# Optimization experiments

Hardware: AMD Instinct MI355X
Metric: run time of the kernel (lower is better)

Reference implementation:

```python
import jax, jax.numpy as jnp
import numpy as np

CENTER_RADIUS = 2.5
TOPK = 13
IOU_WEIGHT = 3.0
BETA = 2.0
NUM_CLASSES = 80
BBOX_W = 2.0
BIG = 1e8
EPS = 1e-7
IMG = 1280


def pairwise_iou(boxes, gts):
    # boxes [N,4], gts [M,4] xyxy -> [N,M]
    lt = jnp.maximum(boxes[:, None, :2], gts[None, :, :2])
    rb = jnp.minimum(boxes[:, None, 2:], gts[None, :, 2:])
    wh = jnp.clip(rb - lt, 0.0)
    inter = wh[..., 0] * wh[..., 1]
    area_a = (boxes[:, 2] - boxes[:, 0]) * (boxes[:, 3] - boxes[:, 1])
    area_b = (gts[:, 2] - gts[:, 0]) * (gts[:, 3] - gts[:, 1])
    union = area_a[:, None] + area_b[None, :] - inter
    return inter / jnp.maximum(union, EPS)


def giou_elementwise(a, b):
    # a,b [N,4] xyxy -> [N]
    lt = jnp.maximum(a[:, :2], b[:, :2])
    rb = jnp.minimum(a[:, 2:], b[:, 2:])
    wh = jnp.clip(rb - lt, 0.0)
    inter = wh[:, 0] * wh[:, 1]
    area_a = (a[:, 2] - a[:, 0]) * (a[:, 3] - a[:, 1])
    area_b = (b[:, 2] - b[:, 0]) * (b[:, 3] - b[:, 1])
    union = area_a + area_b - inter
    iou = inter / jnp.maximum(union, EPS)
    elt = jnp.minimum(a[:, :2], b[:, :2])
    erb = jnp.maximum(a[:, 2:], b[:, 2:])
    ewh = jnp.clip(erb - elt, 0.0)
    enclose = ewh[:, 0] * ewh[:, 1]
    return iou - (enclose - union) / jnp.maximum(enclose, EPS)


def simota_assign(pred_scores, pred_boxes, points, strides, gt_boxes, gt_labels):
    N = points.shape[0]
    M = gt_boxes.shape[0]
    px, py = points[:, 0], points[:, 1]
    # Step 1: candidate selection (inside box OR inside center region)
    in_box = ((px[:, None] > gt_boxes[None, :, 0]) & (py[:, None] > gt_boxes[None, :, 1]) &
              (px[:, None] < gt_boxes[None, :, 2]) & (py[:, None] < gt_boxes[None, :, 3]))
    gcx = (gt_boxes[:, 0] + gt_boxes[:, 2]) * 0.5
    gcy = (gt_boxes[:, 1] + gt_boxes[:, 3]) * 0.5
    r = CENTER_RADIUS * strides[:, None]
    in_center = ((px[:, None] > gcx[None, :] - r) & (py[:, None] > gcy[None, :] - r) &
                 (px[:, None] < gcx[None, :] + r) & (py[:, None] < gcy[None, :] + r))
    is_cand = in_box | in_center          # [N,M]
    cand_any = is_cand.any(axis=1)        # [N]
    # Step 2: cost = BCE(prob, onehot) + w * (-log IoU)
    iou = pairwise_iou(pred_boxes, gt_boxes)  # [N,M]
    p = jnp.clip(pred_scores, 1e-6, 1.0 - 1e-6)
    log_p = jnp.log(p)
    log_1mp = jnp.log1p(-p)
    all_neg = -log_1mp.sum(axis=-1)       # [N] sum_c BCE(p_c, 0)
    cls_cost = all_neg[:, None] + log_1mp[:, gt_labels] - log_p[:, gt_labels]
    reg_cost = -jnp.log(iou + EPS)
    cost = cls_cost + IOU_WEIGHT * reg_cost
    cost = jnp.where(is_cand, cost, BIG)
    # Step 3: dynamic k from top-k IoUs over candidate points (candidates of any gt)
    iou_cand = jnp.where(cand_any[:, None], iou, 0.0)
    topk_ious, _ = jax.lax.top_k(iou_cand.T, TOPK)            # [M,TOPK]
    dyn_k = jnp.clip(topk_ious.sum(axis=-1).astype(jnp.int32), 1, None)  # [M], <= TOPK
    # Step 4: per-gt lowest-cost candidates; k_j entries, only valid (cost < BIG)
    neg_top, top_idx = jax.lax.top_k(-cost.T, TOPK)           # [M,TOPK]
    top_cost = -neg_top
    ranks = jnp.arange(TOPK)
    select = (ranks[None, :] < dyn_k[:, None]) & (top_cost < BIG)
    matching = jnp.zeros((N, M), bool).at[top_idx, jnp.arange(M)[:, None]].set(select)
    # Step 5: conflict resolution -> keep lowest-cost gt per point
    matched = matching.any(axis=1)
    best = jnp.argmin(jnp.where(matching, cost, jnp.inf), axis=1)  # [N]
    rows = jnp.arange(N)
    labels = jnp.where(matched, gt_labels[best], NUM_CLASSES)
    aboxes = jnp.where(matched[:, None], gt_boxes[best], 0.0)
    pos_iou = jnp.where(matched, iou[rows, best], 0.0)
    ascores = jnp.zeros((N, NUM_CLASSES), pred_scores.dtype).at[rows, gt_labels[best]].set(pos_iou)
    return labels, aboxes, ascores


def reference(pred_logits, pred_boxes, points, strides, gt_boxes, gt_labels):
    pred_scores = jax.nn.sigmoid(pred_logits)
    sg = jax.lax.stop_gradient
    labels, aboxes, ascores = simota_assign(sg(pred_scores), sg(pred_boxes),
                                            sg(points), sg(strides), sg(gt_boxes), gt_labels)
    labels, aboxes, ascores = sg(labels), sg(aboxes), sg(ascores)
    # Quality Focal Loss
    x, t = pred_logits, ascores
    bce = jnp.maximum(x, 0.0) - x * t + jnp.log1p(jnp.exp(-jnp.abs(x)))
    scale = jnp.abs(t - pred_scores) ** BETA
    n_pos_cls = jnp.maximum(1, (t > 0).sum()).astype(x.dtype)
    loss_cls = (scale * bce).sum() / n_pos_cls
    # GIoU loss over positives
    matched = labels < NUM_CLASSES
    g = giou_elementwise(pred_boxes, aboxes)
    n_pos = jnp.maximum(1, matched.sum()).astype(x.dtype)
    loss_box = jnp.where(matched, 1.0 - g, 0.0).sum() / n_pos
    return loss_cls + BBOX_W * loss_box


def setup_inputs() -> dict:
    key = jax.random.key(0)
    k1, k2, k3, k4, k5 = jax.random.split(key, 5)
    # multi-scale grid points for a 1280x1280 image, strides 8/16/32
    pts, strs = [], []
    for s in (8, 16, 32):
        n = IMG // s
        c = (jnp.arange(n, dtype=jnp.float32) + 0.5) * s
        yy, xx = jnp.meshgrid(c, c, indexing='ij')
        pts.append(jnp.stack([xx.ravel(), yy.ravel()], axis=-1))
        strs.append(jnp.full((n * n,), float(s), jnp.float32))
    points = jnp.concatenate(pts, axis=0)          # [33600,2]
    strides = jnp.concatenate(strs, axis=0)        # [33600]
    N = points.shape[0]
    pred_logits = jax.random.normal(k1, (N, NUM_CLASSES), jnp.float32) - 2.0
    # decode-style boxes: point +/- positive ltrb distances
    d = jax.random.uniform(k2, (N, 4), jnp.float32) * 64.0 + 1.0
    pred_boxes = jnp.stack([points[:, 0] - d[:, 0], points[:, 1] - d[:, 1],
                            points[:, 0] + d[:, 2], points[:, 1] + d[:, 3]], axis=-1)
    M = 256
    c = jax.random.uniform(k3, (M, 2), jnp.float32) * IMG
    wh = jax.random.uniform(k4, (M, 2), jnp.float32) * 200.0 + 8.0
    gt_boxes = jnp.concatenate([jnp.clip(c - wh / 2, 0, IMG), jnp.clip(c + wh / 2, 0, IMG)], axis=-1)
    gt_labels = jax.random.randint(k5, (M,), 0, NUM_CLASSES, jnp.int32)
    return {"pred_logits": pred_logits, "pred_boxes": pred_boxes, "points": points,
            "strides": strides, "gt_boxes": gt_boxes, "gt_labels": gt_labels}
```

## Files before the change

kernel.cpp:

```cpp
#include <hip/hip_runtime.h>
#include <cstdint>
#include <math.h>

#define NCLS 80
#define TKK 13
#define BIGC 100000000.0f
#define EPSC 1e-7f
#define CRAD 2.5f
#define MARGIN 66.0f
#define XCLP 13.815511f
#define AW 8

__device__ __constant__ int   c_ln[3]   = {160, 80, 40};
__device__ __constant__ float c_ls[3]   = {8.0f, 16.0f, 32.0f};
__device__ __constant__ int   c_lbase[3]= {0, 25600, 32000};

__device__ __forceinline__ void sig_sp(float x, float& s, float& sp){
    float e = __expf(-fabsf(x));
    float L = __logf(1.0f + e);
    sp = fmaxf(x, 0.0f) + L;
    s = __fdividef((x >= 0.0f) ? 1.0f : e, 1.0f + e);
}

__global__ __launch_bounds__(256) void k_prep(
    const float* __restrict__ logits, const float* __restrict__ gt,
    int M, int N, int nbA,
    unsigned long long* __restrict__ best, char* __restrict__ cand,
    float* __restrict__ comb_t, double* __restrict__ base_cls,
    double* __restrict__ accd, int* __restrict__ acci)
{
    int b = blockIdx.x;
    if (b < nbA){
        __shared__ float t[64][81];
        __shared__ float s_an[64];
        int tid = threadIdx.x;
        if (b == 0 && tid == 0){
            accd[0] = 0.0; accd[1] = 0.0;
            acci[0] = 0; acci[1] = 0; acci[2] = 0;
        }
        int nl = tid >> 2, p = tid & 3;
        int n = b * 64 + nl;
        const float4* lg4 = (const float4*)(logits + (size_t)n * NCLS + p * 20);
        float xs[20];
        float an = 0.0f;
        double bc = 0.0;
        #pragma unroll
        for (int q = 0; q < 5; q++){
            float4 v = lg4[q];
            xs[q*4+0] = v.x; xs[q*4+1] = v.y; xs[q*4+2] = v.z; xs[q*4+3] = v.w;
            #pragma unroll
            for (int k = 0; k < 4; k++){
                float x = xs[q*4+k];
                float s, sp;
                sig_sp(x, s, sp);
                an += fminf(sp, XCLP);
                bc += (double)((s * s) * sp);
            }
        }
        #pragma unroll
        for (int q = 0; q < 20; q++) t[nl][p * 20 + q] = xs[q];
        an += __shfl_down(an, 2, 4);
        an += __shfl_down(an, 1, 4);
        bc += __shfl_down(bc, 2, 4);
        bc += __shfl_down(bc, 1, 4);
        if (p == 0){
            s_an[nl] = an;
            base_cls[n] = bc;
            best[n] = 0xFFFFFFFFFFFFFFFFull;
        }
        __syncthreads();
        int lane = tid & 63, wv = tid >> 6;
        int n0 = b * 64;
        float av = s_an[lane];
        #pragma unroll 5
        for (int it = 0; it < 20; it++){
            int c = it * 4 + wv;
            float x = t[lane][c];
            float xc = fminf(fmaxf(x, -XCLP), XCLP);
            comb_t[(size_t)c * N + n0 + lane] = av - xc;
        }
    } else {
        int m = b - nbA;
        int tid = threadIdx.x;
        float gx0 = gt[4*m], gy0 = gt[4*m+1], gx1 = gt[4*m+2], gy1 = gt[4*m+3];
        float cx = (gx0 + gx1) * 0.5f, cy = (gy0 + gy1) * 0.5f;
        for (int lvl = 0; lvl < 3; lvl++){
            int   ng = c_ln[lvl];
            float s  = c_ls[lvl];
            int   base = c_lbase[lvl];
            float r = CRAD * s;
            float xlo = fminf(gx0, cx - r), xhi = fmaxf(gx1, cx + r);
            float ylo = fminf(gy0, cy - r), yhi = fmaxf(gy1, cy + r);
            int j0 = max(0, (int)floorf(xlo / s - 0.5f));
            int j1 = min(ng - 1, (int)ceilf(xhi / s - 0.5f));
            int i0 = max(0, (int)floorf(ylo / s - 0.5f));
            int i1 = min(ng - 1, (int)ceilf(yhi / s - 0.5f));
            if (j1 < j0 || i1 < i0) continue;
            int w = j1 - j0 + 1;
            int cells = w * (i1 - i0 + 1);
            for (int c = tid; c < cells; c += 256){
                int ii = i0 + c / w, jj = j0 + c % w;
                float px = (jj + 0.5f) * s, py = (ii + 0.5f) * s;
                bool ib = (px > gx0) && (py > gy0) && (px < gx1) && (py < gy1);
                bool ic = (px > cx - r) && (py > cy - r) && (px < cx + r) && (py < cy + r);
                if (ib || ic) cand[base + ii * ng + jj] = 1;
            }
        }
    }
}

__global__ __launch_bounds__(512) void k_assign(
    const float* __restrict__ pboxes, const float* __restrict__ comb_t,
    const float* __restrict__ gt, const int* __restrict__ glab,
    const char* __restrict__ cand,
    unsigned long long* __restrict__ best, int N)
{
    int m = blockIdx.x;
    int tid = threadIdx.x;
    int lane = tid & 63, wv = tid >> 6;

    float gx0 = gt[4*m], gy0 = gt[4*m+1], gx1 = gt[4*m+2], gy1 = gt[4*m+3];
    float areaB = (gx1 - gx0) * (gy1 - gy0);
    float cx = (gx0 + gx1) * 0.5f, cy = (gy0 + gy1) * 0.5f;
    int lab = glab[m];
    const float* __restrict__ combrow = comb_t + (size_t)lab * N;

    float liou[TKK];
    float lc[TKK]; int li[TKK];
    #pragma unroll
    for (int r = 0; r < TKK; r++){ liou[r] = 0.0f; lc[r] = INFINITY; li[r] = 0x7fffffff; }

    for (int lvl = 0; lvl < 3; lvl++){
        int   ng = c_ln[lvl];
        float s  = c_ls[lvl];
        int   base = c_lbase[lvl];
        float r = CRAD * s;
        float xlo = fminf(gx0 - MARGIN, cx - r), xhi = fmaxf(gx1 + MARGIN, cx + r);
        float ylo = fminf(gy0 - MARGIN, cy - r), yhi = fmaxf(gy1 + MARGIN, cy + r);
        int j0 = max(0, (int)floorf(xlo / s - 0.5f));
        int j1 = min(ng - 1, (int)ceilf(xhi / s - 0.5f));
        int i0 = max(0, (int)floorf(ylo / s - 0.5f));
        int i1 = min(ng - 1, (int)ceilf(yhi / s - 0.5f));
        if (j1 < j0 || i1 < i0) continue;
        int w = j1 - j0 + 1;
        int cells = w * (i1 - i0 + 1);
        for (int cb = wv * 64; cb < cells; cb += 2048){
            #pragma unroll
            for (int k = 0; k < 4; k++){
                int c = cb + k * 512 + lane;
                if (c >= cells) continue;
                int ii = i0 + (int)((unsigned)c / (unsigned)w);
                int jj = j0 + (int)((unsigned)c % (unsigned)w);
                int n = base + ii * ng + jj;

                float4 pb = ((const float4*)pboxes)[n];
                float comb = combrow[n];
                char  cd   = cand[n];

                float ltx = fmaxf(pb.x, gx0), lty = fmaxf(pb.y, gy0);
                float rbx = fminf(pb.z, gx1), rby = fminf(pb.w, gy1);
                float ww = fmaxf(rbx - ltx, 0.0f), hh = fmaxf(rby - lty, 0.0f);
                float inter = ww * hh;
                float areaA = (pb.z - pb.x) * (pb.w - pb.y);
                float uni = areaA + areaB - inter;
                float iou = inter / fmaxf(uni, EPSC);

                float ioum = (cd == 1) ? iou : 0.0f;
                if (ioum > liou[TKK-1]){
                    float v = ioum;
                    #pragma unroll
                    for (int j = 0; j < TKK; j++){
                        float a = liou[j];
                        bool ins = (v > a);
                        liou[j] = ins ? v : a;
                        v = ins ? a : v;
                    }
                }

                float px = (jj + 0.5f) * s, py = (ii + 0.5f) * s;
                bool ib = (px > gx0) && (py > gy0) && (px < gx1) && (py < gy1);
                bool ic = (px > cx - r) && (py > cy - r) && (px < cx + r) && (py < cy + r);
                float cost = comb + 3.0f * (-__logf(iou + EPSC));
                bool top = (ib || ic) &&
                           ((cost < lc[TKK-1]) || (cost == lc[TKK-1] && n < li[TKK-1]));
                if (top){
                    float v = cost; int ix = n;
                    #pragma unroll
                    for (int j = 0; j < TKK; j++){
                        float a = lc[j]; int ai = li[j];
                        bool ins = (v < a) || (v == a && ix < ai);
                        lc[j] = ins ? v : a;  li[j] = ins ? ix : ai;
                        v = ins ? a : v;      ix = ins ? ai : ix;
                    }
                }
            }
        }
    }

    __shared__ float s_iou[AW*TKK];
    __shared__ float s_cv[AW*TKK];
    __shared__ int   s_ci[AW*TKK];
    __shared__ float s_topc[TKK];
    __shared__ int   s_topi[TKK];
    __shared__ int   s_dynk;

    for (int r = 0; r < TKK; r++){
        float v = liou[0]; int o = lane;
        #pragma unroll
        for (int off = 32; off > 0; off >>= 1){
            float ov = __shfl_down(v, off);
            int   oo = __shfl_down(o, off);
            if (ov > v){ v = ov; o = oo; }
        }
        v = __shfl(v, 0); o = __shfl(o, 0);
        if (lane == 0) s_iou[wv*TKK + r] = v;
        if (v <= 0.0f){
            if (lane == 0) for (int rr = r+1; rr < TKK; rr++) s_iou[wv*TKK + rr] = 0.0f;
            break;
        }
        if (lane == o){
            #pragma unroll
            for (int j = 0; j < TKK-1; j++) liou[j] = liou[j+1];
            liou[TKK-1] = 0.0f;
        }
    }
    for (int r = 0; r < TKK; r++){
        float v = lc[0]; int ix = li[0]; int o = lane;
        #pragma unroll
        for (int off = 32; off > 0; off >>= 1){
            float ov = __shfl_down(v, off);
            int  oix = __shfl_down(ix, off);
            int   oo = __shfl_down(o, off);
            if (ov < v || (ov == v && oix < ix)){ v = ov; ix = oix; o = oo; }
        }
        v = __shfl(v, 0); ix = __shfl(ix, 0); o = __shfl(o, 0);
        if (lane == 0){ s_cv[wv*TKK + r] = v; s_ci[wv*TKK + r] = ix; }
        if (v == INFINITY){
            if (lane == 0) for (int rr = r+1; rr < TKK; rr++){
                s_cv[wv*TKK + rr] = INFINITY; s_ci[wv*TKK + rr] = 0x7fffffff;
            }
            break;
        }
        if (lane == o){
            #pragma unroll
            for (int j = 0; j < TKK-1; j++){ lc[j] = lc[j+1]; li[j] = li[j+1]; }
            lc[TKK-1] = INFINITY; li[TKK-1] = 0x7fffffff;
        }
    }
    __syncthreads();

    if (wv == 0){
        float v0 = (lane < AW*TKK) ? s_iou[lane] : 0.0f;
        float v1 = (64 + lane < AW*TKK) ? s_iou[64 + lane] : 0.0f;
        float isum = 0.0f;
        for (int r = 0; r < TKK; r++){
            float x = fmaxf(v0, v1);
            int o = lane;
            #pragma unroll
            for (int off = 32; off > 0; off >>= 1){
                float ox = __shfl_down(x, off);
                int   oo = __shfl_down(o, off);
                if (ox > x){ x = ox; o = oo; }
            }
            x = __shfl(x, 0); o = __shfl(o, 0);
            if (x <= 0.0f) break;
            isum += x;
            if (lane == o){
                if (v0 == x) v0 = 0.0f;
                else         v1 = 0.0f;
            }
        }
        if (lane == 0){
            int dynk = (int)isum;
            if (dynk < 1) dynk = 1;
            if (dynk > TKK) dynk = TKK;
            s_dynk = dynk;
        }
    } else if (wv == 1){
        float c0, c1; int i0_, i1_;
        if (lane < AW*TKK){ c0 = s_cv[lane]; i0_ = s_ci[lane]; }
        else { c0 = INFINITY; i0_ = 0x7fffffff; }
        if (64 + lane < AW*TKK){ c1 = s_cv[64 + lane]; i1_ = s_ci[64 + lane]; }
        else { c1 = INFINITY; i1_ = 0x7fffffff; }
        for (int r = 0; r < TKK; r++){
            bool p0 = (c0 < c1) || (c0 == c1 && i0_ < i1_);
            float x = p0 ? c0 : c1;
            int  xi = p0 ? i0_ : i1_;
            int o = lane;
            #pragma unroll
            for (int off = 32; off > 0; off >>= 1){
                float ox = __shfl_down(x, off);
                int  oxi = __shfl_down(xi, off);
                int   oo = __shfl_down(o, off);
                if (ox < x || (ox == x && oxi < xi)){ x = ox; xi = oxi; o = oo; }
            }
            x = __shfl(x, 0); xi = __shfl(xi, 0); o = __shfl(o, 0);
            if (lane == 0){ s_topc[r] = x; s_topi[r] = xi; }
            if (x == INFINITY){
                if (lane == 0) for (int rr = r+1; rr < TKK; rr++){
                    s_topc[rr] = INFINITY; s_topi[rr] = 0x7fffffff;
                }
                break;
            }
            if (lane == o){
                if (c0 == x && i0_ == xi){ c0 = INFINITY; i0_ = 0x7fffffff; }
                else                     { c1 = INFINITY; i1_ = 0x7fffffff; }
            }
        }
    }
    __syncthreads();

    if (tid < s_dynk){
        float c = s_topc[tid];
        int   i = s_topi[tid];
        if (c < BIGC && i < 0x7fffffff){
            unsigned u = __float_as_uint(c);
            u = (u & 0x80000000u) ? ~u : (u | 0x80000000u);
            unsigned long long key = ((unsigned long long)u << 32) | (unsigned)m;
            atomicMin(best + i, key);
        }
    }
}

__global__ __launch_bounds__(256) void k_loss(
    const float* __restrict__ logits, const float* __restrict__ pboxes,
    const float* __restrict__ gt, const int* __restrict__ glab,
    const unsigned long long* __restrict__ best,
    const double* __restrict__ base_cls,
    double* __restrict__ accd, int* __restrict__ acci,
    int N, int nblocks, float* __restrict__ out)
{
    int n = blockIdx.x * 256 + threadIdx.x;
    int tid = threadIdx.x;
    int lane = tid & 63, wv = tid >> 6;
    double scls = 0.0, sbox = 0.0;
    int cm = 0, cp = 0;

    if (n < N){
        scls = base_cls[n];
        unsigned long long b = best[n];
        if (b != 0xFFFFFFFFFFFFFFFFull){
            int m = (int)(b & 0xFFFFFFFFu);
            int lab = glab[m];
            float4 pb = ((const float4*)pboxes)[n];
            float gx0 = gt[4*m], gy0 = gt[4*m+1], gx1 = gt[4*m+2], gy1 = gt[4*m+3];
            float ltx = fmaxf(pb.x, gx0), lty = fmaxf(pb.y, gy0);
            float rbx = fminf(pb.z, gx1), rby = fminf(pb.w, gy1);
            float w = fmaxf(rbx - ltx, 0.0f), h = fmaxf(rby - lty, 0.0f);
            float inter = w * h;
            float areaA = (pb.z - pb.x) * (pb.w - pb.y);
            float areaB = (gx1 - gx0) * (gy1 - gy0);
            float uni = areaA + areaB - inter;
            float iou = inter / fmaxf(uni, EPSC);
            float eltx = fminf(pb.x, gx0), elty = fminf(pb.y, gy0);
            float erbx = fmaxf(pb.z, gx1), erby = fmaxf(pb.w, gy1);
            float ew = fmaxf(erbx - eltx, 0.0f), eh = fmaxf(erby - elty, 0.0f);
            float enc = ew * eh;
            float giou = iou - (enc - uni) / fmaxf(enc, EPSC);
            sbox = (double)(1.0f - giou);
            cm = 1;
            cp = (iou > 0.0f) ? 1 : 0;
            float x = logits[(size_t)n * NCLS + lab];
            float s, spv;
            sig_sp(x, s, spv);
            float bcet = spv - x * iou;
            float d = iou - s;
            scls = scls - (double)((s * s) * spv) + (double)((d * d) * bcet);
        }
    }

    #pragma unroll
    for (int off = 32; off > 0; off >>= 1){
        scls += __shfl_down(scls, off);
        sbox += __shfl_down(sbox, off);
        cm   += __shfl_down(cm, off);
        cp   += __shfl_down(cp, off);
    }
    __shared__ double sd0[4];
    __shared__ double sd1[4];
    __shared__ int    si0[4];
    __shared__ int    si1[4];
    if (lane == 0){ sd0[wv] = scls; sd1[wv] = sbox; si0[wv] = cm; si1[wv] = cp; }
    __syncthreads();
    if (tid == 0){
        double a0 = 0.0, a1 = 0.0; int c0 = 0, c1 = 0;
        #pragma unroll
        for (int q = 0; q < 4; q++){ a0 += sd0[q]; a1 += sd1[q]; c0 += si0[q]; c1 += si1[q]; }
        atomicAdd(&accd[0], a0);
        atomicAdd(&accd[1], a1);
        atomicAdd(&acci[0], c0);
        atomicAdd(&acci[1], c1);
        __threadfence();
        int donec = atomicAdd(&acci[2], 1);
        if (donec == nblocks - 1){
            double A0 = atomicAdd(&accd[0], 0.0);
            double A1 = atomicAdd(&accd[1], 0.0);
            int C0 = atomicAdd(&acci[0], 0);
            int C1 = atomicAdd(&acci[1], 0);
            if (C0 < 1) C0 = 1;
            if (C1 < 1) C1 = 1;
            out[0] = (float)(A0 / (double)C1 + 2.0 * A1 / (double)C0);
        }
    }
}

extern "C" void kernel_launch(void* const* d_in, const int* in_sizes, int n_in,
                              void* d_out, int out_size, void* d_ws, size_t ws_size,
                              hipStream_t stream) {
    const float* logits  = (const float*)d_in[0];
    const float* pboxes  = (const float*)d_in[1];
    const float* gtb     = (const float*)d_in[4];
    const int*   glab    = (const int*)d_in[5];

    int N = in_sizes[3];
    int M = in_sizes[5];

    char* ws = (char*)d_ws;
    size_t off = 0;
    unsigned long long* best = (unsigned long long*)(ws + off); off += (size_t)8 * N;
    double* base_cls = (double*)(ws + off); off += (size_t)8 * N;
    float*  comb_t   = (float*)(ws + off);  off += (size_t)4 * NCLS * N;
    char*   cand = (char*)(ws + off);       off += (size_t)N;
    off = (off + 15) & ~(size_t)15;
    double* accd = (double*)(ws + off);     off += 16;
    int*    acci = (int*)(ws + off);        off += 16;

    int nbA = N / 64;
    int nbL = (N + 255) / 256;
    k_prep<<<nbA + M, 256, 0, stream>>>(logits, gtb, M, N, nbA,
                                        best, cand, comb_t, base_cls, accd, acci);
    k_assign<<<M, 512, 0, stream>>>(pboxes, comb_t, gtb, glab, cand, best, N);
    k_loss<<<nbL, 256, 0, stream>>>(logits, pboxes, gtb, glab, best, base_cls,
                                    accd, acci, N, nbL, (float*)d_out);
}
```

Before: 117.1 us.

## Fuse loss reduction into assign kernel via software grid barrier

Removes the separate k_loss launch. After the top-k assignment, each k_assign block waits at a spin-based grid barrier on an atomic counter, then computes the per-anchor loss for a 512-anchor slice and accumulates it. A second counter picks the last block to finish, which writes the final output. This saves one kernel launch and its dependency gap. In exchange, correctness depends on all M blocks being resident on the GPU at the same time, and the spin-wait adds sync overhead.

```diff
diff --git a/kernel.cpp b/kernel.cpp
--- a/kernel.cpp
+++ b/kernel.cpp
@@ -36,7 +36,7 @@
         int tid = threadIdx.x;
         if (b == 0 && tid == 0){
             accd[0] = 0.0; accd[1] = 0.0;
-            acci[0] = 0; acci[1] = 0; acci[2] = 0;
+            acci[0] = 0; acci[1] = 0; acci[2] = 0; acci[3] = 0;
         }
         int nl = tid >> 2, p = tid & 3;
         int n = b * 64 + nl;
@@ -113,7 +113,9 @@
     const float* __restrict__ pboxes, const float* __restrict__ comb_t,
     const float* __restrict__ gt, const int* __restrict__ glab,
     const char* __restrict__ cand,
-    unsigned long long* __restrict__ best, int N)
+    unsigned long long* __restrict__ best, int N, int M,
+    const float* __restrict__ logits, const double* __restrict__ base_cls,
+    double* __restrict__ accd, int* __restrict__ acci, float* __restrict__ out)
 {
     int m = blockIdx.x;
     int tid = threadIdx.x;
@@ -320,47 +322,44 @@
             atomicMin(best + i, key);
         }
     }
-}
-
-__global__ __launch_bounds__(256) void k_loss(
-    const float* __restrict__ logits, const float* __restrict__ pboxes,
-    const float* __restrict__ gt, const int* __restrict__ glab,
-    const unsigned long long* __restrict__ best,
-    const double* __restrict__ base_cls,
-    double* __restrict__ accd, int* __restrict__ acci,
-    int N, int nblocks, float* __restrict__ out)
-{
-    int n = blockIdx.x * 256 + threadIdx.x;
-    int tid = threadIdx.x;
-    int lane = tid & 63, wv = tid >> 6;
+    __syncthreads();
+
+    if (tid == 0){
+        __threadfence();
+        atomicAdd(&acci[2], 1);
+        while (atomicAdd(&acci[2], 0) < M){ __builtin_amdgcn_s_sleep(1); }
+    }
+    __syncthreads();
+    __threadfence();
+
+    int n = m * 512 + tid;
     double scls = 0.0, sbox = 0.0;
     int cm = 0, cp = 0;
-
     if (n < N){
         scls = base_cls[n];
-        unsigned long long b = best[n];
+        unsigned long long b = atomicMin(best + n, 0xFFFFFFFFFFFFFFFFull);
         if (b != 0xFFFFFFFFFFFFFFFFull){
-            int m = (int)(b & 0xFFFFFFFFu);
-            int lab = glab[m];
+            int bm = (int)(b & 0xFFFFFFFFu);
+            int blab = glab[bm];
             float4 pb = ((const float4*)pboxes)[n];
-            float gx0 = gt[4*m], gy0 = gt[4*m+1], gx1 = gt[4*m+2], gy1 = gt[4*m+3];
-            float ltx = fmaxf(pb.x, gx0), lty = fmaxf(pb.y, gy0);
-            float rbx = fminf(pb.z, gx1), rby = fminf(pb.w, gy1);
+            float bx0 = gt[4*bm], by0 = gt[4*bm+1], bx1 = gt[4*bm+2], by1 = gt[4*bm+3];
+            float ltx = fmaxf(pb.x, bx0), lty = fmaxf(pb.y, by0);
+            float rbx = fminf(pb.z, bx1), rby = fminf(pb.w, by1);
             float w = fmaxf(rbx - ltx, 0.0f), h = fmaxf(rby - lty, 0.0f);
             float inter = w * h;
             float areaA = (pb.z - pb.x) * (pb.w - pb.y);
-            float areaB = (gx1 - gx0) * (gy1 - gy0);
-            float uni = areaA + areaB - inter;
+            float areaB2 = (bx1 - bx0) * (by1 - by0);
+            float uni = areaA + areaB2 - inter;
             float iou = inter / fmaxf(uni, EPSC);
-            float eltx = fminf(pb.x, gx0), elty = fminf(pb.y, gy0);
-            float erbx = fmaxf(pb.z, gx1), erby = fmaxf(pb.w, gy1);
+            float eltx = fminf(pb.x, bx0), elty = fminf(pb.y, by0);
+            float erbx = fmaxf(pb.z, bx1), erby = fmaxf(pb.w, by1);
             float ew = fmaxf(erbx - eltx, 0.0f), eh = fmaxf(erby - elty, 0.0f);
             float enc = ew * eh;
             float giou = iou - (enc - uni) / fmaxf(enc, EPSC);
             sbox = (double)(1.0f - giou);
             cm = 1;
             cp = (iou > 0.0f) ? 1 : 0;
-            float x = logits[(size_t)n * NCLS + lab];
+            float x = logits[(size_t)n * NCLS + blab];
             float s, spv;
             sig_sp(x, s, spv);
             float bcet = spv - x * iou;
@@ -376,23 +375,23 @@
         cm   += __shfl_down(cm, off);
         cp   += __shfl_down(cp, off);
     }
-    __shared__ double sd0[4];
-    __shared__ double sd1[4];
-    __shared__ int    si0[4];
-    __shared__ int    si1[4];
+    __shared__ double sd0[AW];
+    __shared__ double sd1[AW];
+    __shared__ int    si0[AW];
+    __shared__ int    si1[AW];
     if (lane == 0){ sd0[wv] = scls; sd1[wv] = sbox; si0[wv] = cm; si1[wv] = cp; }
     __syncthreads();
     if (tid == 0){
         double a0 = 0.0, a1 = 0.0; int c0 = 0, c1 = 0;
         #pragma unroll
-        for (int q = 0; q < 4; q++){ a0 += sd0[q]; a1 += sd1[q]; c0 += si0[q]; c1 += si1[q]; }
+        for (int q = 0; q < AW; q++){ a0 += sd0[q]; a1 += sd1[q]; c0 += si0[q]; c1 += si1[q]; }
         atomicAdd(&accd[0], a0);
         atomicAdd(&accd[1], a1);
         atomicAdd(&acci[0], c0);
         atomicAdd(&acci[1], c1);
         __threadfence();
-        int donec = atomicAdd(&acci[2], 1);
-        if (donec == nblocks - 1){
+        int donec = atomicAdd(&acci[3], 1);
+        if (donec == M - 1){
             double A0 = atomicAdd(&accd[0], 0.0);
             double A1 = atomicAdd(&accd[1], 0.0);
             int C0 = atomicAdd(&acci[0], 0);
@@ -426,10 +425,8 @@
     int*    acci = (int*)(ws + off);        off += 16;
 
     int nbA = N / 64;
-    int nbL = (N + 255) / 256;
     k_prep<<<nbA + M, 256, 0, stream>>>(logits, gtb, M, N, nbA,
                                         best, cand, comb_t, base_cls, accd, acci);
-    k_assign<<<M, 512, 0, stream>>>(pboxes, comb_t, gtb, glab, cand, best, N);
-    k_loss<<<nbL, 256, 0, stream>>>(logits, pboxes, gtb, glab, best, base_cls,
-                                    accd, acci, N, nbL, (float*)d_out);
+    k_assign<<<M, 512, 0, stream>>>(pboxes, comb_t, gtb, glab, cand, best, N, M,
+                                    logits, base_cls, accd, acci, (float*)d_out);
 }
```

Result: slower. 162.4 us (+38.7%).
